# Performance work log

Measured on AMD Instinct MI355X. Metric: run time of the kernel, lower is better.

The kernel has to match this reference:

```python
import jax, jax.numpy as jnp
import numpy as np

B, D, K1, N = 64, 128, 4096, 100000  # batch, feat dim, K+1 samples, memory rows
T_TEMP = 0.07
MOMENTUM = 0.5


def setup_inputs() -> dict:
    key = jax.random.key(0)
    ks = jax.random.split(key, 24)
    stdv = 1.0 / np.sqrt(D / 3.0)
    w_scale = 1.0 / np.sqrt(D)
    v1 = jax.random.normal(ks[0], (B, D), dtype=jnp.float32)
    v2 = jax.random.normal(ks[1], (B, D), dtype=jnp.float32)
    y = jax.random.randint(ks[2], (B,), 0, N)
    idx = jax.random.randint(ks[3], (B, K1), 0, N)
    idx = idx.at[:, 0].set(y)  # first sample is the positive
    memory_v2 = jax.random.uniform(ks[4], (N, D), dtype=jnp.float32, minval=-stdv, maxval=stdv)

    def lin(k):
        kw, kb = jax.random.split(k)
        return (jax.random.uniform(kw, (D, D), dtype=jnp.float32, minval=-w_scale, maxval=w_scale),
                jax.random.uniform(kb, (D,), dtype=jnp.float32, minval=-w_scale, maxval=w_scale))

    mt_w1, mt_b1 = lin(ks[5]); mt_w2, mt_b2 = lin(ks[6]); mt_wv, mt_bv = lin(ks[7])
    mts_w1, mts_b1 = lin(ks[8]); mts_w2, mts_b2 = lin(ks[9]); mts_wv, mts_bv = lin(ks[10])
    ht_w, ht_b = lin(ks[11]); hts_w, hts_b = lin(ks[12])
    return dict(v1=v1, v2=v2, memory_v2=memory_v2,
                mt_w1=mt_w1, mt_b1=mt_b1, mt_w2=mt_w2, mt_b2=mt_b2, mt_wv=mt_wv, mt_bv=mt_bv,
                mts_w1=mts_w1, mts_b1=mts_b1, mts_w2=mts_w2, mts_b2=mts_b2, mts_wv=mts_wv, mts_bv=mts_bv,
                ht_w=ht_w, ht_b=ht_b, hts_w=hts_w, hts_b=hts_b, y=y, idx=idx)


def _sync_embed(x, w, w1, b1, w2, b2, wv, bv, hw, hb):
    # x: [B,D] anchor feature; w: [S,B,D] gathered memory samples
    a = x @ w1.T + b1                                  # [B,D]
    b = jnp.einsum('sbd,ed->sbe', w, w2) + b2          # [S,B,D]
    pre = jax.nn.relu(a[None, :, :] - b)               # Synchronize: relu(W1 v1 - W2 v2)
    h = jnp.einsum('sbd,ed->sbe', pre, wv) + bv        # v(...)
    h = jnp.einsum('sbd,ed->sbe', h, hw) + hb          # Embed linear
    return h / jnp.sqrt(jnp.sum(h * h, axis=-1, keepdims=True))  # l2norm


def reference(v1, v2, memory_v2,
              mt_w1, mt_b1, mt_w2, mt_b2, mt_wv, mt_bv,
              mts_w1, mts_b1, mts_w2, mts_b2, mts_wv, mts_bv,
              ht_w, ht_b, hts_w, hts_b, y, idx):
    # gather negatives/positive from memory bank: [B,K+1,D] -> [K+1,B,D]
    w = jnp.swapaxes(memory_v2[idx], 0, 1)
    outs_m_t = _sync_embed(v2, w, mt_w1, mt_b1, mt_w2, mt_b2, mt_wv, mt_bv, ht_w, ht_b)
    outs_m_t_s = _sync_embed(v1, w, mts_w1, mts_b1, mts_w2, mts_b2, mts_wv, mts_bv, hts_w, hts_b)
    score = jnp.exp(jnp.sum(outs_m_t * outs_m_t_s, axis=2, keepdims=True) / T_TEMP) / jnp.exp(1.0 / T_TEMP)
    # momentum scatter update of memory bank (no_grad in original)
    ab = memory_v2[y] * MOMENTUM + v2 * (1.0 - MOMENTUM)
    ab = ab / jnp.sqrt(jnp.sum(ab * ab, axis=1, keepdims=True))
    new_memory = memory_v2.at[y].set(ab)
    return score, new_memory
```

## Files before the change

kernel.cpp:

```cpp
#include <hip/hip_runtime.h>
#include <hip/hip_fp16.h>

typedef __attribute__((ext_vector_type(8))) _Float16 f16x8;
typedef __attribute__((ext_vector_type(4))) float f32x4;
typedef __attribute__((ext_vector_type(4))) unsigned short u16x4;
typedef unsigned short u16;
typedef unsigned int u32;

#define MFMA16F(a,b,c) __builtin_amdgcn_mfma_f32_16x16x32_f16(a,b,c,0,0,0)

__device__ __forceinline__ u16 f16rn(float x){
  return (u16)__half_as_ushort(__float2half(x));
}

__device__ __forceinline__ void gload_lds16(const void* g, void* l){
  __builtin_amdgcn_global_load_lds((const __attribute__((address_space(1))) u32*)g,
                                   (__attribute__((address_space(3))) u32*)l, 16, 0, 0);
}

__global__ __launch_bounds__(128) void prep_kernel(
    const float* __restrict__ v1, const float* __restrict__ v2,
    const float* __restrict__ mt_w1, const float* __restrict__ mt_b1,
    const float* __restrict__ mt_w2, const float* __restrict__ mt_b2,
    const float* __restrict__ mt_wv, const float* __restrict__ mt_bv,
    const float* __restrict__ mts_w1, const float* __restrict__ mts_b1,
    const float* __restrict__ mts_w2, const float* __restrict__ mts_b2,
    const float* __restrict__ mts_wv, const float* __restrict__ mts_bv,
    const float* __restrict__ ht_w, const float* __restrict__ ht_b,
    const float* __restrict__ hts_w, const float* __restrict__ hts_b,
    u16* __restrict__ w2a, u16* __restrict__ w2b,
    u16* __restrict__ wc1, u16* __restrict__ wc2,
    float* __restrict__ c1, float* __restrict__ c2,
    float* __restrict__ bc1, float* __restrict__ bc2)
{
  const int blk = blockIdx.x;
  const int t = threadIdx.x;
  if (blk < 128) {
    const bool second = blk >= 64;
    const int b = blk & 63;
    const float* x  = second ? v1 : v2;
    const float* w1 = second ? mts_w1 : mt_w1;
    const float* b1 = second ? mts_b1 : mt_b1;
    const float* b2 = second ? mts_b2 : mt_b2;
    float* c = second ? c2 : c1;
    __shared__ float xr[128];
    xr[t] = x[b*128 + t];
    __syncthreads();
    float s = 0.f;
    #pragma unroll 8
    for (int k=0;k<128;k++) s += w1[t*128 + k] * xr[k];
    c[b*128 + t] = s + b1[t] - b2[t];
  } else if (blk < 384) {
    const bool second = blk >= 256;
    const int e = blk - (second ? 256 : 128);
    const float* hw = second ? hts_w : ht_w;
    const float* wv = second ? mts_wv : mt_wv;
    const float* bv = second ? mts_bv : mt_bv;
    const float* hb = second ? hts_b : ht_b;
    u16* wc = second ? wc2 : wc1;
    float* bcp = second ? bc2 : bc1;
    float s = 0.f;
    #pragma unroll 8
    for (int k=0;k<128;k++) s += hw[e*128 + k] * wv[k*128 + t];
    wc[e*128 + t] = f16rn(s);
    __shared__ float red[128];
    red[t] = hw[e*128 + t] * bv[t];
    __syncthreads();
    for (int off=64; off>0; off>>=1){ if (t<off) red[t] += red[t+off]; __syncthreads(); }
    if (t==0) bcp[e] = red[0] + hb[e];
  } else {
    const int i = (blk-384)*128 + t;
    w2a[i] = f16rn(mt_w2[i]);
    w2b[i] = f16rn(mts_w2[i]);
  }
}

__global__ __launch_bounds__(512, 2) void main_kernel(
    const u16* __restrict__ mp,
    const int* __restrict__ idx,
    const u16* __restrict__ w2a, const u16* __restrict__ w2b,
    const u16* __restrict__ wc1, const u16* __restrict__ wc2,
    const float* __restrict__ c1, const float* __restrict__ c2,
    const float* __restrict__ bc1, const float* __restrict__ bc2,
    float* __restrict__ wss)
{
  __shared__ u16 Mbuf[2][64*128];
  __shared__ u16 P1[64*128], P2[64*128];
  __shared__ float part[8][64][3];

  const int tid  = threadIdx.x;
  const int wid  = tid >> 6;
  const int lane = tid & 63;
  const int lg = lane >> 4, li = lane & 15;

  const int wbase = (wid*16 + li)*128 + lg*8;
  f16x8 W2a[4], W2b[4], Vca[4], Vcb[4];
  #pragma unroll
  for (int k=0;k<4;k++){
    W2a[k] = *(const f16x8*)(w2a + wbase + k*32);
    W2b[k] = *(const f16x8*)(w2b + wbase + k*32);
    Vca[k] = *(const f16x8*)(wc1 + wbase + k*32);
    Vcb[k] = *(const f16x8*)(wc2 + wbase + k*32);
  }

  const int bid = blockIdx.x;
  const int b = bid >> 4;
  const int sbase = (bid & 15) * 256;

  const int q = lane >> 4, sl = lane & 15;
  u32 goff[4][2];
  #pragma unroll
  for (int I=0;I<4;I++){
    #pragma unroll
    for (int j=0;j<2;j++){
      const int grow = wid*8 + j*4 + q;
      const int ridx = idx[b*4096 + sbase + I*64 + grow];
      goff[I][j] = (u32)ridx*128 + (u32)((sl ^ (grow&15))*8);
    }
  }

  #define DO_GATHER(I, BUF) {                                        \
    _Pragma("unroll")                                                \
    for (int j=0;j<2;j++)                                            \
      gload_lds16(mp + goff[I][j], &Mbuf[BUF][(wid*8 + j*4)*128]);   \
  }

  #define SCORE_OUT(I) {                                             \
    if (tid < 64){                                                   \
      float S11=0.f, S22=0.f, S12=0.f;                               \
      _Pragma("unroll")                                              \
      for (int w=0; w<8; w++){                                       \
        S11 += part[w][tid][0]; S22 += part[w][tid][1]; S12 += part[w][tid][2]; \
      }                                                              \
      float dot = S12 / sqrtf(S11 * S22);                            \
      wss[(size_t)b*4096 + sbase + (I)*64 + tid] = expf((dot - 1.0f) * (1.0f/0.07f)); \
    }                                                                \
  }

  DO_GATHER(0, 0);
  DO_GATHER(1, 1);

  #pragma unroll
  for (int i=0; i<4; ++i){
    if (i < 3) asm volatile("s_waitcnt vmcnt(2) lgkmcnt(0)" ::: "memory");
    else       asm volatile("s_waitcnt vmcnt(0) lgkmcnt(0)" ::: "memory");
    __builtin_amdgcn_s_barrier();
    __builtin_amdgcn_sched_barrier(0);

    if (i >= 1) SCORE_OUT(i-1);

    const u16* mc = &Mbuf[i&1][0];

    f32x4 A1[4], A2[4];
    #pragma unroll
    for (int n=0;n<4;n++){ A1[n]=(f32x4)(0.f); A2[n]=(f32x4)(0.f); }
    #pragma unroll
    for (int k=0;k<4;k++){
      __builtin_amdgcn_s_setprio(1);
      #pragma unroll
      for (int n=0;n<4;n++){
        const int a = (n*16+li)*128 + (((k*4+lg) ^ li)<<3);
        f16x8 bh = *(const f16x8*)(mc + a);
        A1[n] = MFMA16F(W2a[k], bh, A1[n]);
        A2[n] = MFMA16F(W2b[k], bh, A2[n]);
      }
      __builtin_amdgcn_s_setprio(0);
    }

    {
      const float4 cv1 = *(const float4*)(c1 + b*128 + wid*16 + lg*4);
      const float4 cv2 = *(const float4*)(c2 + b*128 + wid*16 + lg*4);
      const int c = wid*2 + (lg>>1);
      const int sub = (lg&1)*4;
      #pragma unroll
      for (int n=0;n<4;n++){
        const int row = n*16 + li;
        const int a2 = row*128 + ((c ^ li)<<3) + sub;
        u16x4 h4, g4;
        #pragma unroll
        for (int r=0;r<4;r++){
          float c1r = (r==0)?cv1.x:(r==1)?cv1.y:(r==2)?cv1.z:cv1.w;
          float c2r = (r==0)?cv2.x:(r==1)?cv2.y:(r==2)?cv2.z:cv2.w;
          h4[r] = f16rn(fmaxf(c1r - A1[n][r], 0.f));
          g4[r] = f16rn(fmaxf(c2r - A2[n][r], 0.f));
        }
        *(u16x4*)&P1[a2] = h4;
        *(u16x4*)&P2[a2] = g4;
      }
    }
    asm volatile("s_waitcnt lgkmcnt(0)" ::: "memory");
    __builtin_amdgcn_s_barrier();
    __builtin_amdgcn_sched_barrier(0);

    if (i < 2) DO_GATHER(i+2, i&1);

    #pragma unroll
    for (int n=0;n<4;n++){ A1[n]=(f32x4)(0.f); A2[n]=(f32x4)(0.f); }
    #pragma unroll
    for (int k=0;k<4;k++){
      __builtin_amdgcn_s_setprio(1);
      #pragma unroll
      for (int n=0;n<4;n++){
        const int a = (n*16+li)*128 + (((k*4+lg) ^ li)<<3);
        f16x8 p1h = *(const f16x8*)(P1 + a);
        f16x8 p2h = *(const f16x8*)(P2 + a);
        A1[n] = MFMA16F(Vca[k], p1h, A1[n]);
        A2[n] = MFMA16F(Vcb[k], p2h, A2[n]);
      }
      __builtin_amdgcn_s_setprio(0);
    }

    {
      const float4 bb1 = *(const float4*)(bc1 + wid*16 + lg*4);
      const float4 bb2 = *(const float4*)(bc2 + wid*16 + lg*4);
      #pragma unroll
      for (int n=0;n<4;n++){
        float p11=0.f, p22=0.f, p12=0.f;
        #pragma unroll
        for (int r=0;r<4;r++){
          float e1 = (r==0)?bb1.x:(r==1)?bb1.y:(r==2)?bb1.z:bb1.w;
          float e2 = (r==0)?bb2.x:(r==1)?bb2.y:(r==2)?bb2.z:bb2.w;
          float v1h = A1[n][r] + e1;
          float v2h = A2[n][r] + e2;
          p11 += v1h*v1h; p22 += v2h*v2h; p12 += v1h*v2h;
        }
        p11 += __shfl_xor(p11, 16, 64); p11 += __shfl_xor(p11, 32, 64);
        p22 += __shfl_xor(p22, 16, 64); p22 += __shfl_xor(p22, 32, 64);
        p12 += __shfl_xor(p12, 16, 64); p12 += __shfl_xor(p12, 32, 64);
        if (lane < 16){
          part[wid][n*16+li][0] = p11;
          part[wid][n*16+li][1] = p22;
          part[wid][n*16+li][2] = p12;
        }
      }
    }
  }

  asm volatile("s_waitcnt lgkmcnt(0)" ::: "memory");
  __builtin_amdgcn_s_barrier();
  __builtin_amdgcn_sched_barrier(0);
  SCORE_OUT(3);

  #undef DO_GATHER
  #undef SCORE_OUT
}

__global__ __launch_bounds__(256) void split_copy_kernel(const float4* __restrict__ src,
    float4* __restrict__ dst, u16x4* __restrict__ mp4, int n4, int docopy)
{
  int i = blockIdx.x*256 + threadIdx.x;
  const int stride = gridDim.x*256;
  for (; i < n4; i += stride){
    float4 f = src[i];
    if (docopy) dst[i] = f;
    u16x4 h;
    h[0] = f16rn(f.x); h[1] = f16rn(f.y); h[2] = f16rn(f.z); h[3] = f16rn(f.w);
    mp4[i] = h;
  }
}

__global__ __launch_bounds__(256) void copy_kernel(const float4* __restrict__ src,
                                                   float4* __restrict__ dst, int n4)
{
  int i = blockIdx.x*256 + threadIdx.x;
  const int stride = gridDim.x*256;
  for (; i < n4; i += stride) dst[i] = src[i];
}

__global__ __launch_bounds__(128) void update_kernel(const float* __restrict__ mem,
    const float* __restrict__ v2, const int* __restrict__ y, float* __restrict__ outmem)
{
  const int b = blockIdx.x;
  const int t = threadIdx.x;
  const int row = y[b];
  for (int b2=b+1; b2<64; ++b2) if (y[b2] == row) return;
  float ab = 0.5f*mem[(size_t)row*128 + t] + 0.5f*v2[b*128 + t];
  __shared__ float red[2];
  float s = ab*ab;
  #pragma unroll
  for (int off=1; off<64; off<<=1) s += __shfl_xor(s, off, 64);
  if ((t & 63) == 0) red[t>>6] = s;
  __syncthreads();
  float tot = red[0] + red[1];
  outmem[(size_t)row*128 + t] = ab / sqrtf(tot);
}

__global__ __launch_bounds__(256) void transpose_kernel(const float* __restrict__ wss,
                                                        float* __restrict__ out)
{
  __shared__ float tile[64][65];
  const int t = blockIdx.x;
  const int c = threadIdx.x & 63;
  const int r4 = threadIdx.x >> 6;
  #pragma unroll
  for (int i=0;i<16;i++){
    int bb = i*4 + r4;
    tile[bb][c] = wss[(size_t)bb*4096 + t*64 + c];
  }
  __syncthreads();
  #pragma unroll
  for (int i=0;i<16;i++){
    int s = i*4 + r4;
    out[(size_t)(t*64+s)*64 + c] = tile[c][s];
  }
}

extern "C" void kernel_launch(void* const* d_in, const int* in_sizes, int n_in,
                              void* d_out, int out_size, void* d_ws, size_t ws_size,
                              hipStream_t stream) {
  (void)in_sizes; (void)n_in; (void)out_size;
  const float* v1      = (const float*)d_in[0];
  const float* v2      = (const float*)d_in[1];
  const float* mem     = (const float*)d_in[2];
  const float* mt_w1   = (const float*)d_in[3];
  const float* mt_b1   = (const float*)d_in[4];
  const float* mt_w2   = (const float*)d_in[5];
  const float* mt_b2   = (const float*)d_in[6];
  const float* mt_wv   = (const float*)d_in[7];
  const float* mt_bv   = (const float*)d_in[8];
  const float* mts_w1  = (const float*)d_in[9];
  const float* mts_b1  = (const float*)d_in[10];
  const float* mts_w2  = (const float*)d_in[11];
  const float* mts_b2  = (const float*)d_in[12];
  const float* mts_wv  = (const float*)d_in[13];
  const float* mts_bv  = (const float*)d_in[14];
  const float* ht_w    = (const float*)d_in[15];
  const float* ht_b    = (const float*)d_in[16];
  const float* hts_w   = (const float*)d_in[17];
  const float* hts_b   = (const float*)d_in[18];
  const int*   y       = (const int*)d_in[19];
  const int*   idx     = (const int*)d_in[20];
  float* out = (float*)d_out;
  float* outmem = out + 262144;
  char* ws = (char*)d_ws;

  u16* w2a = (u16*)(ws + 0);
  u16* w2b = (u16*)(ws + 32768);
  u16* wc1 = (u16*)(ws + 65536);
  u16* wc2 = (u16*)(ws + 98304);
  float* c1   = (float*)(ws + 131072);
  float* c2   = (float*)(ws + 163840);
  float* bc1  = (float*)(ws + 196608);
  float* bc2  = (float*)(ws + 197120);
  float* wss  = (float*)(ws + 262144);

  const size_t PLANES_OFF = 2097152;
  const size_t PLANES_BYTES = (size_t)100000 * 128 * 2;
  const bool bigws = ws_size >= PLANES_OFF + PLANES_BYTES;
  u16* mp = bigws ? (u16*)(ws + PLANES_OFF) : (u16*)outmem;

  split_copy_kernel<<<2048, 256, 0, stream>>>((const float4*)mem, (float4*)outmem,
                                              (u16x4*)mp, 3200000, bigws ? 1 : 0);
  prep_kernel<<<512, 128, 0, stream>>>(v1, v2,
      mt_w1, mt_b1, mt_w2, mt_b2, mt_wv, mt_bv,
      mts_w1, mts_b1, mts_w2, mts_b2, mts_wv, mts_bv,
      ht_w, ht_b, hts_w, hts_b,
      w2a, w2b, wc1, wc2, c1, c2, bc1, bc2);
  main_kernel<<<1024, 512, 0, stream>>>(mp, idx,
      w2a, w2b, wc1, wc2, c1, c2, bc1, bc2, wss);
  if (!bigws)
    copy_kernel<<<2048, 256, 0, stream>>>((const float4*)mem, (float4*)outmem, 3200000);
  update_kernel<<<64, 128, 0, stream>>>(mem, v2, y, outmem);
  transpose_kernel<<<64, 256, 0, stream>>>(wss, out);
}
```

Before: 100.2 us.

## Use 4-wave blocks with two output tiles per wave in main kernel

The main kernel moves from 512-thread blocks (8 waves, 16 output features each) to 256-thread blocks (4 waves, 32 features each via two M sub-tiles). Each LDS B-fragment load now feeds four MFMAs instead of two, and the grid doubles to 2048 blocks of 128 samples with only two gather stages. The aim is more MFMA work per LDS read and smaller blocks for scheduling. The cost is higher register pressure from doubled weight fragments and accumulators, and less gather prefetch depth per block.

```diff
diff --git a/kernel.cpp b/kernel.cpp
--- a/kernel.cpp
+++ b/kernel.cpp
@@ -75,7 +75,7 @@
   }
 }
 
-__global__ __launch_bounds__(512, 2) void main_kernel(
+__global__ __launch_bounds__(256, 2) void main_kernel(
     const u16* __restrict__ mp,
     const int* __restrict__ idx,
     const u16* __restrict__ w2a, const u16* __restrict__ w2b,
@@ -86,51 +86,63 @@
 {
   __shared__ u16 Mbuf[2][64*128];
   __shared__ u16 P1[64*128], P2[64*128];
-  __shared__ float part[8][64][3];
+  __shared__ float part[4][64][3];
 
   const int tid  = threadIdx.x;
-  const int wid  = tid >> 6;
+  const int w    = tid >> 6;
   const int lane = tid & 63;
   const int lg = lane >> 4, li = lane & 15;
 
-  const int wbase = (wid*16 + li)*128 + lg*8;
-  f16x8 W2a[4], W2b[4], Vca[4], Vcb[4];
-  #pragma unroll
-  for (int k=0;k<4;k++){
-    W2a[k] = *(const f16x8*)(w2a + wbase + k*32);
-    W2b[k] = *(const f16x8*)(w2b + wbase + k*32);
-    Vca[k] = *(const f16x8*)(wc1 + wbase + k*32);
-    Vcb[k] = *(const f16x8*)(wc2 + wbase + k*32);
+  f16x8 W2a[2][4], W2b[2][4], Vca[2][4], Vcb[2][4];
+  #pragma unroll
+  for (int mm=0;mm<2;mm++){
+    const int wb = (w*32 + mm*16 + li)*128 + lg*8;
+    #pragma unroll
+    for (int k=0;k<4;k++){
+      W2a[mm][k] = *(const f16x8*)(w2a + wb + k*32);
+      W2b[mm][k] = *(const f16x8*)(w2b + wb + k*32);
+      Vca[mm][k] = *(const f16x8*)(wc1 + wb + k*32);
+      Vcb[mm][k] = *(const f16x8*)(wc2 + wb + k*32);
+    }
   }
 
   const int bid = blockIdx.x;
-  const int b = bid >> 4;
-  const int sbase = (bid & 15) * 256;
+  const int b = bid >> 5;
+  const int sbase = (bid & 31) * 128;
+
+  float4 cv1[2], cv2[2], bb1[2], bb2[2];
+  #pragma unroll
+  for (int mm=0;mm<2;mm++){
+    cv1[mm] = *(const float4*)(c1 + b*128 + w*32 + mm*16 + lg*4);
+    cv2[mm] = *(const float4*)(c2 + b*128 + w*32 + mm*16 + lg*4);
+    bb1[mm] = *(const float4*)(bc1 + w*32 + mm*16 + lg*4);
+    bb2[mm] = *(const float4*)(bc2 + w*32 + mm*16 + lg*4);
+  }
 
   const int q = lane >> 4, sl = lane & 15;
-  u32 goff[4][2];
-  #pragma unroll
-  for (int I=0;I<4;I++){
-    #pragma unroll
-    for (int j=0;j<2;j++){
-      const int grow = wid*8 + j*4 + q;
+  u32 goff[2][4];
+  #pragma unroll
+  for (int I=0;I<2;I++){
+    #pragma unroll
+    for (int j=0;j<4;j++){
+      const int grow = w*16 + j*4 + q;
       const int ridx = idx[b*4096 + sbase + I*64 + grow];
-      goff[I][j] = (u32)ridx*128 + (u32)((sl ^ (grow&15))*8);
+      goff[I][j] = (u32)ridx*128 + (u32)((sl ^ (j*4+q))*8);
     }
   }
 
   #define DO_GATHER(I, BUF) {                                        \
     _Pragma("unroll")                                                \
-    for (int j=0;j<2;j++)                                            \
-      gload_lds16(mp + goff[I][j], &Mbuf[BUF][(wid*8 + j*4)*128]);   \
+    for (int j=0;j<4;j++)                                            \
+      gload_lds16(mp + goff[I][j], &Mbuf[BUF][(w*16 + j*4)*128]);    \
   }
 
   #define SCORE_OUT(I) {                                             \
     if (tid < 64){                                                   \
       float S11=0.f, S22=0.f, S12=0.f;                               \
       _Pragma("unroll")                                              \
-      for (int w=0; w<8; w++){                                       \
-        S11 += part[w][tid][0]; S22 += part[w][tid][1]; S12 += part[w][tid][2]; \
+      for (int ww=0; ww<4; ww++){                                    \
+        S11 += part[ww][tid][0]; S22 += part[ww][tid][1]; S12 += part[ww][tid][2]; \
       }                                                              \
       float dot = S12 / sqrtf(S11 * S22);                            \
       wss[(size_t)b*4096 + sbase + (I)*64 + tid] = expf((dot - 1.0f) * (1.0f/0.07f)); \
@@ -141,19 +153,21 @@
   DO_GATHER(1, 1);
 
   #pragma unroll
-  for (int i=0; i<4; ++i){
-    if (i < 3) asm volatile("s_waitcnt vmcnt(2) lgkmcnt(0)" ::: "memory");
-    else       asm volatile("s_waitcnt vmcnt(0) lgkmcnt(0)" ::: "memory");
+  for (int i=0; i<2; ++i){
+    if (i == 0) asm volatile("s_waitcnt vmcnt(4) lgkmcnt(0)" ::: "memory");
+    else        asm volatile("s_waitcnt vmcnt(0) lgkmcnt(0)" ::: "memory");
     __builtin_amdgcn_s_barrier();
     __builtin_amdgcn_sched_barrier(0);
 
     if (i >= 1) SCORE_OUT(i-1);
 
-    const u16* mc = &Mbuf[i&1][0];
-
-    f32x4 A1[4], A2[4];
-    #pragma unroll
-    for (int n=0;n<4;n++){ A1[n]=(f32x4)(0.f); A2[n]=(f32x4)(0.f); }
+    const u16* mc = &Mbuf[i][0];
+
+    f32x4 A1[2][4], A2[2][4];
+    #pragma unroll
+    for (int mm=0;mm<2;mm++)
+      #pragma unroll
+      for (int n=0;n<4;n++){ A1[mm][n]=(f32x4)(0.f); A2[mm][n]=(f32x4)(0.f); }
     #pragma unroll
     for (int k=0;k<4;k++){
       __builtin_amdgcn_s_setprio(1);
@@ -161,28 +175,30 @@
       for (int n=0;n<4;n++){
         const int a = (n*16+li)*128 + (((k*4+lg) ^ li)<<3);
         f16x8 bh = *(const f16x8*)(mc + a);
-        A1[n] = MFMA16F(W2a[k], bh, A1[n]);
-        A2[n] = MFMA16F(W2b[k], bh, A2[n]);
+        #pragma unroll
+        for (int mm=0;mm<2;mm++){
+          A1[mm][n] = MFMA16F(W2a[mm][k], bh, A1[mm][n]);
+          A2[mm][n] = MFMA16F(W2b[mm][k], bh, A2[mm][n]);
+        }
       }
       __builtin_amdgcn_s_setprio(0);
     }
 
-    {
-      const float4 cv1 = *(const float4*)(c1 + b*128 + wid*16 + lg*4);
-      const float4 cv2 = *(const float4*)(c2 + b*128 + wid*16 + lg*4);
-      const int c = wid*2 + (lg>>1);
+    #pragma unroll
+    for (int mm=0;mm<2;mm++){
+      const int g = w*4 + mm*2 + (lg>>1);
       const int sub = (lg&1)*4;
       #pragma unroll
       for (int n=0;n<4;n++){
         const int row = n*16 + li;
-        const int a2 = row*128 + ((c ^ li)<<3) + sub;
+        const int a2 = row*128 + ((g ^ li)<<3) + sub;
         u16x4 h4, g4;
         #pragma unroll
         for (int r=0;r<4;r++){
-          float c1r = (r==0)?cv1.x:(r==1)?cv1.y:(r==2)?cv1.z:cv1.w;
-          float c2r = (r==0)?cv2.x:(r==1)?cv2.y:(r==2)?cv2.z:cv2.w;
-          h4[r] = f16rn(fmaxf(c1r - A1[n][r], 0.f));
-          g4[r] = f16rn(fmaxf(c2r - A2[n][r], 0.f));
+          float c1r = (r==0)?cv1[mm].x:(r==1)?cv1[mm].y:(r==2)?cv1[mm].z:cv1[mm].w;
+          float c2r = (r==0)?cv2[mm].x:(r==1)?cv2[mm].y:(r==2)?cv2[mm].z:cv2[mm].w;
+          h4[r] = f16rn(fmaxf(c1r - A1[mm][n][r], 0.f));
+          g4[r] = f16rn(fmaxf(c2r - A2[mm][n][r], 0.f));
         }
         *(u16x4*)&P1[a2] = h4;
         *(u16x4*)&P2[a2] = g4;
@@ -192,10 +208,10 @@
     __builtin_amdgcn_s_barrier();
     __builtin_amdgcn_sched_barrier(0);
 
-    if (i < 2) DO_GATHER(i+2, i&1);
-
-    #pragma unroll
-    for (int n=0;n<4;n++){ A1[n]=(f32x4)(0.f); A2[n]=(f32x4)(0.f); }
+    #pragma unroll
+    for (int mm=0;mm<2;mm++)
+      #pragma unroll
+      for (int n=0;n<4;n++){ A1[mm][n]=(f32x4)(0.f); A2[mm][n]=(f32x4)(0.f); }
     #pragma unroll
     for (int k=0;k<4;k++){
       __builtin_amdgcn_s_setprio(1);
@@ -204,34 +220,36 @@
         const int a = (n*16+li)*128 + (((k*4+lg) ^ li)<<3);
         f16x8 p1h = *(const f16x8*)(P1 + a);
         f16x8 p2h = *(const f16x8*)(P2 + a);
-        A1[n] = MFMA16F(Vca[k], p1h, A1[n]);
-        A2[n] = MFMA16F(Vcb[k], p2h, A2[n]);
+        #pragma unroll
+        for (int mm=0;mm<2;mm++){
+          A1[mm][n] = MFMA16F(Vca[mm][k], p1h, A1[mm][n]);
+          A2[mm][n] = MFMA16F(Vcb[mm][k], p2h, A2[mm][n]);
+        }
       }
       __builtin_amdgcn_s_setprio(0);
     }
 
-    {
-      const float4 bb1 = *(const float4*)(bc1 + wid*16 + lg*4);
-      const float4 bb2 = *(const float4*)(bc2 + wid*16 + lg*4);
-      #pragma unroll
-      for (int n=0;n<4;n++){
-        float p11=0.f, p22=0.f, p12=0.f;
+    #pragma unroll
+    for (int n=0;n<4;n++){
+      float p11=0.f, p22=0.f, p12=0.f;
+      #pragma unroll
+      for (int mm=0;mm<2;mm++){
         #pragma unroll
         for (int r=0;r<4;r++){
-          float e1 = (r==0)?bb1.x:(r==1)?bb1.y:(r==2)?bb1.z:bb1.w;
-          float e2 = (r==0)?bb2.x:(r==1)?bb2.y:(r==2)?bb2.z:bb2.w;
-          float v1h = A1[n][r] + e1;
-          float v2h = A2[n][r] + e2;
+          float e1 = (r==0)?bb1[mm].x:(r==1)?bb1[mm].y:(r==2)?bb1[mm].z:bb1[mm].w;
+          float e2 = (r==0)?bb2[mm].x:(r==1)?bb2[mm].y:(r==2)?bb2[mm].z:bb2[mm].w;
+          float v1h = A1[mm][n][r] + e1;
+          float v2h = A2[mm][n][r] + e2;
           p11 += v1h*v1h; p22 += v2h*v2h; p12 += v1h*v2h;
         }
-        p11 += __shfl_xor(p11, 16, 64); p11 += __shfl_xor(p11, 32, 64);
-        p22 += __shfl_xor(p22, 16, 64); p22 += __shfl_xor(p22, 32, 64);
-        p12 += __shfl_xor(p12, 16, 64); p12 += __shfl_xor(p12, 32, 64);
-        if (lane < 16){
-          part[wid][n*16+li][0] = p11;
-          part[wid][n*16+li][1] = p22;
-          part[wid][n*16+li][2] = p12;
-        }
+      }
+      p11 += __shfl_xor(p11, 16, 64); p11 += __shfl_xor(p11, 32, 64);
+      p22 += __shfl_xor(p22, 16, 64); p22 += __shfl_xor(p22, 32, 64);
+      p12 += __shfl_xor(p12, 16, 64); p12 += __shfl_xor(p12, 32, 64);
+      if (lane < 16){
+        part[w][n*16+li][0] = p11;
+        part[w][n*16+li][1] = p22;
+        part[w][n*16+li][2] = p12;
       }
     }
   }
@@ -239,7 +257,7 @@
   asm volatile("s_waitcnt lgkmcnt(0)" ::: "memory");
   __builtin_amdgcn_s_barrier();
   __builtin_amdgcn_sched_barrier(0);
-  SCORE_OUT(3);
+  SCORE_OUT(1);
 
   #undef DO_GATHER
   #undef SCORE_OUT
@@ -356,7 +374,7 @@
       mts_w1, mts_b1, mts_w2, mts_b2, mts_wv, mts_bv,
       ht_w, ht_b, hts_w, hts_b,
       w2a, w2b, wc1, wc2, c1, c2, bc1, bc2);
-  main_kernel<<<1024, 512, 0, stream>>>(mp, idx,
+  main_kernel<<<2048, 256, 0, stream>>>(mp, idx,
       w2a, w2b, wc1, wc2, c1, c2, bc1, bc2, wss);
   if (!bigws)
     copy_kernel<<<2048, 256, 0, stream>>>((const float4*)mem, (float4*)outmem, 3200000);
```

Measured after the change: 126.8 us. 1.27x slower.

## Switch main kernel to 32x32x16 MFMA with 2D wave tiling

Applied to the files above, without the earlier changes.

Replaces the 16x16x32 MFMA tiles with 32x32x16 MFMA. Each wave now computes a 32-feature by 32-sample tile (4 feature groups x 2 sample groups) instead of 16 features x 64 samples. This cuts the LDS operand reads per MFMA and the cross-lane shuffle reductions, and halves the partial-sum array. In exchange each wave holds twice as many weight registers (8 fragments per matrix), which raises register pressure at 2 blocks per CU.

```diff
diff --git a/kernel.cpp b/kernel.cpp
--- a/kernel.cpp
+++ b/kernel.cpp
@@ -2,12 +2,12 @@
 #include <hip/hip_fp16.h>
 
 typedef __attribute__((ext_vector_type(8))) _Float16 f16x8;
-typedef __attribute__((ext_vector_type(4))) float f32x4;
+typedef __attribute__((ext_vector_type(16))) float f32x16;
 typedef __attribute__((ext_vector_type(4))) unsigned short u16x4;
 typedef unsigned short u16;
 typedef unsigned int u32;
 
-#define MFMA16F(a,b,c) __builtin_amdgcn_mfma_f32_16x16x32_f16(a,b,c,0,0,0)
+#define MFMA32F(a,b,c) __builtin_amdgcn_mfma_f32_32x32x16_f16(a,b,c,0,0,0)
 
 __device__ __forceinline__ u16 f16rn(float x){
   return (u16)__half_as_ushort(__float2half(x));
@@ -86,21 +86,27 @@
 {
   __shared__ u16 Mbuf[2][64*128];
   __shared__ u16 P1[64*128], P2[64*128];
-  __shared__ float part[8][64][3];
+  __shared__ float part[4][64][3];
 
   const int tid  = threadIdx.x;
   const int wid  = tid >> 6;
   const int lane = tid & 63;
-  const int lg = lane >> 4, li = lane & 15;
-
-  const int wbase = (wid*16 + li)*128 + lg*8;
-  f16x8 W2a[4], W2b[4], Vca[4], Vcb[4];
-  #pragma unroll
-  for (int k=0;k<4;k++){
-    W2a[k] = *(const f16x8*)(w2a + wbase + k*32);
-    W2b[k] = *(const f16x8*)(w2b + wbase + k*32);
-    Vca[k] = *(const f16x8*)(wc1 + wbase + k*32);
-    Vcb[k] = *(const f16x8*)(wc2 + wbase + k*32);
+  const int l31 = lane & 31;
+  const int l15 = lane & 15;
+  const int h   = lane >> 5;
+  const int dg  = wid >> 1;
+  const int sg  = wid & 1;
+
+  f16x8 W2a[8], W2b[8], Vca[8], Vcb[8];
+  {
+    const int wb = (dg*32 + l31)*128 + h*8;
+    #pragma unroll
+    for (int kk=0;kk<8;kk++){
+      W2a[kk] = *(const f16x8*)(w2a + wb + kk*16);
+      W2b[kk] = *(const f16x8*)(w2b + wb + kk*16);
+      Vca[kk] = *(const f16x8*)(wc1 + wb + kk*16);
+      Vcb[kk] = *(const f16x8*)(wc2 + wb + kk*16);
+    }
   }
 
   const int bid = blockIdx.x;
@@ -129,8 +135,8 @@
     if (tid < 64){                                                   \
       float S11=0.f, S22=0.f, S12=0.f;                               \
       _Pragma("unroll")                                              \
-      for (int w=0; w<8; w++){                                       \
-        S11 += part[w][tid][0]; S22 += part[w][tid][1]; S12 += part[w][tid][2]; \
+      for (int g_=0; g_<4; g_++){                                    \
+        S11 += part[g_][tid][0]; S22 += part[g_][tid][1]; S12 += part[g_][tid][2]; \
       }                                                              \
       float dot = S12 / sqrtf(S11 * S22);                            \
       wss[(size_t)b*4096 + sbase + (I)*64 + tid] = expf((dot - 1.0f) * (1.0f/0.07f)); \
@@ -139,6 +145,8 @@
 
   DO_GATHER(0, 0);
   DO_GATHER(1, 1);
+
+  const int rbase = (sg*32 + l31)*128;
 
   #pragma unroll
   for (int i=0; i<4; ++i){
@@ -151,41 +159,36 @@
 
     const u16* mc = &Mbuf[i&1][0];
 
-    f32x4 A1[4], A2[4];
+    f32x16 A1 = (f32x16)(0.f), A2 = (f32x16)(0.f);
+    __builtin_amdgcn_s_setprio(1);
     #pragma unroll
-    for (int n=0;n<4;n++){ A1[n]=(f32x4)(0.f); A2[n]=(f32x4)(0.f); }
-    #pragma unroll
-    for (int k=0;k<4;k++){
-      __builtin_amdgcn_s_setprio(1);
+    for (int kk=0;kk<8;kk++){
+      const int a = rbase + (((kk*2 + h) ^ l15)<<3);
+      f16x8 bh = *(const f16x8*)(mc + a);
+      A1 = MFMA32F(W2a[kk], bh, A1);
+      A2 = MFMA32F(W2b[kk], bh, A2);
+    }
+    __builtin_amdgcn_s_setprio(0);
+
+    {
+      const float* c1L = c1 + (size_t)b*128;
+      const float* c2L = c2 + (size_t)b*128;
+      asm volatile("" : "+v"(c1L), "+v"(c2L));
       #pragma unroll
-      for (int n=0;n<4;n++){
-        const int a = (n*16+li)*128 + (((k*4+lg) ^ li)<<3);
-        f16x8 bh = *(const f16x8*)(mc + a);
-        A1[n] = MFMA16F(W2a[k], bh, A1[n]);
-        A2[n] = MFMA16F(W2b[k], bh, A2[n]);
-      }
-      __builtin_amdgcn_s_setprio(0);
-    }
-
-    {
-      const float4 cv1 = *(const float4*)(c1 + b*128 + wid*16 + lg*4);
-      const float4 cv2 = *(const float4*)(c2 + b*128 + wid*16 + lg*4);
-      const int c = wid*2 + (lg>>1);
-      const int sub = (lg&1)*4;
-      #pragma unroll
-      for (int n=0;n<4;n++){
-        const int row = n*16 + li;
-        const int a2 = row*128 + ((c ^ li)<<3) + sub;
+      for (int g=0; g<4; g++){
+        const float4 cv1 = *(const float4*)(c1L + dg*32 + 8*g + 4*h);
+        const float4 cv2 = *(const float4*)(c2L + dg*32 + 8*g + 4*h);
         u16x4 h4, g4;
         #pragma unroll
         for (int r=0;r<4;r++){
           float c1r = (r==0)?cv1.x:(r==1)?cv1.y:(r==2)?cv1.z:cv1.w;
           float c2r = (r==0)?cv2.x:(r==1)?cv2.y:(r==2)?cv2.z:cv2.w;
-          h4[r] = f16rn(fmaxf(c1r - A1[n][r], 0.f));
-          g4[r] = f16rn(fmaxf(c2r - A2[n][r], 0.f));
+          h4[r] = f16rn(fmaxf(c1r - A1[g*4+r], 0.f));
+          g4[r] = f16rn(fmaxf(c2r - A2[g*4+r], 0.f));
         }
-        *(u16x4*)&P1[a2] = h4;
-        *(u16x4*)&P2[a2] = g4;
+        const int aw = rbase + (((dg*4+g) ^ l15)<<3) + h*4;
+        *(u16x4*)&P1[aw] = h4;
+        *(u16x4*)&P2[aw] = g4;
       }
     }
     asm volatile("s_waitcnt lgkmcnt(0)" ::: "memory");
@@ -194,44 +197,43 @@
 
     if (i < 2) DO_GATHER(i+2, i&1);
 
+    A1 = (f32x16)(0.f); A2 = (f32x16)(0.f);
+    __builtin_amdgcn_s_setprio(1);
     #pragma unroll
-    for (int n=0;n<4;n++){ A1[n]=(f32x4)(0.f); A2[n]=(f32x4)(0.f); }
-    #pragma unroll
-    for (int k=0;k<4;k++){
-      __builtin_amdgcn_s_setprio(1);
+    for (int kk=0;kk<8;kk++){
+      const int a = rbase + (((kk*2 + h) ^ l15)<<3);
+      f16x8 p1 = *(const f16x8*)(P1 + a);
+      f16x8 p2 = *(const f16x8*)(P2 + a);
+      A1 = MFMA32F(Vca[kk], p1, A1);
+      A2 = MFMA32F(Vcb[kk], p2, A2);
+    }
+    __builtin_amdgcn_s_setprio(0);
+
+    {
+      const float* b1L = bc1;
+      const float* b2L = bc2;
+      asm volatile("" : "+v"(b1L), "+v"(b2L));
+      float p11=0.f, p22=0.f, p12=0.f;
       #pragma unroll
-      for (int n=0;n<4;n++){
-        const int a = (n*16+li)*128 + (((k*4+lg) ^ li)<<3);
-        f16x8 p1h = *(const f16x8*)(P1 + a);
-        f16x8 p2h = *(const f16x8*)(P2 + a);
-        A1[n] = MFMA16F(Vca[k], p1h, A1[n]);
-        A2[n] = MFMA16F(Vcb[k], p2h, A2[n]);
-      }
-      __builtin_amdgcn_s_setprio(0);
-    }
-
-    {
-      const float4 bb1 = *(const float4*)(bc1 + wid*16 + lg*4);
-      const float4 bb2 = *(const float4*)(bc2 + wid*16 + lg*4);
-      #pragma unroll
-      for (int n=0;n<4;n++){
-        float p11=0.f, p22=0.f, p12=0.f;
+      for (int g=0; g<4; g++){
+        const float4 e1 = *(const float4*)(b1L + dg*32 + 8*g + 4*h);
+        const float4 e2 = *(const float4*)(b2L + dg*32 + 8*g + 4*h);
         #pragma unroll
         for (int r=0;r<4;r++){
-          float e1 = (r==0)?bb1.x:(r==1)?bb1.y:(r==2)?bb1.z:bb1.w;
-          float e2 = (r==0)?bb2.x:(r==1)?bb2.y:(r==2)?bb2.z:bb2.w;
-          float v1h = A1[n][r] + e1;
-          float v2h = A2[n][r] + e2;
+          float ee1 = (r==0)?e1.x:(r==1)?e1.y:(r==2)?e1.z:e1.w;
+          float ee2 = (r==0)?e2.x:(r==1)?e2.y:(r==2)?e2.z:e2.w;
+          float v1h = A1[g*4+r] + ee1;
+          float v2h = A2[g*4+r] + ee2;
           p11 += v1h*v1h; p22 += v2h*v2h; p12 += v1h*v2h;
         }
-        p11 += __shfl_xor(p11, 16, 64); p11 += __shfl_xor(p11, 32, 64);
-        p22 += __shfl_xor(p22, 16, 64); p22 += __shfl_xor(p22, 32, 64);
-        p12 += __shfl_xor(p12, 16, 64); p12 += __shfl_xor(p12, 32, 64);
-        if (lane < 16){
-          part[wid][n*16+li][0] = p11;
-          part[wid][n*16+li][1] = p22;
-          part[wid][n*16+li][2] = p12;
-        }
+      }
+      p11 += __shfl_xor(p11, 32, 64);
+      p22 += __shfl_xor(p22, 32, 64);
+      p12 += __shfl_xor(p12, 32, 64);
+      if (lane < 32){
+        part[dg][sg*32+lane][0] = p11;
+        part[dg][sg*32+lane][1] = p22;
+        part[dg][sg*32+lane][2] = p12;
       }
     }
   }
```

Result: slower. 113.3 us (+13.1%).
